# Kernel optimization log

Measured on AMD Instinct MI355X. Metric: run time of the kernel, lower is better.

Reference implementation:

```python
import jax, jax.numpy as jnp
import numpy as np

# Mamba block dims (config: d_model=1024, expand=2, d_state=16, d_conv=4, dt_rank=auto)
D_MODEL = 1024
D_INNER = 2048
D_STATE = 16
D_CONV = 4
DT_RANK = 64
B_SZ = 2
SEQ = 2048
EPS = 1e-5
DT_MIN, DT_MAX, DT_FLOOR = 0.001, 0.1, 1e-4


def setup_inputs() -> dict:
    key = jax.random.key(0)
    ks = jax.random.split(key, 8)
    s = 0.02  # initializer_range
    # dt_proj bias init: inverse-softplus of dt sampled log-uniform in [dt_min, dt_max]
    dt = jnp.exp(jax.random.uniform(ks[6], (D_INNER,)) * (np.log(DT_MAX) - np.log(DT_MIN)) + np.log(DT_MIN))
    dt = jnp.clip(dt, DT_FLOOR, None)
    inv_dt = dt + jnp.log(-jnp.expm1(-dt))
    A_init = jnp.broadcast_to(jnp.arange(1, D_STATE + 1, dtype=jnp.float32), (D_INNER, D_STATE))
    return {
        "hidden_states": jax.random.normal(ks[0], (B_SZ, SEQ, D_MODEL), jnp.float32),
        "norm_weight": jnp.ones((D_MODEL,), jnp.float32),
        "in_proj_w": jax.random.normal(ks[1], (2 * D_INNER, D_MODEL), jnp.float32) * s,
        "conv_w": jax.random.normal(ks[2], (D_INNER, 1, D_CONV), jnp.float32) * s,
        "conv_b": jnp.zeros((D_INNER,), jnp.float32),
        "x_proj_w": jax.random.normal(ks[3], (DT_RANK + 2 * D_STATE, D_INNER), jnp.float32) * s,
        "dt_proj_w": jax.random.normal(ks[4], (D_INNER, DT_RANK), jnp.float32) * s,
        "dt_proj_b": inv_dt,
        "A_log": jnp.log(A_init),
        "D": jnp.ones((D_INNER,), jnp.float32),
        "out_proj_w": jax.random.normal(ks[5], (D_MODEL, D_INNER), jnp.float32) * s,
    }


def reference(hidden_states, norm_weight, in_proj_w, conv_w, conv_b, x_proj_w,
              dt_proj_w, dt_proj_b, A_log, D, out_proj_w):
    residual = hidden_states
    # RMSNorm
    h = hidden_states * jax.lax.rsqrt(jnp.mean(hidden_states * hidden_states, -1, keepdims=True) + EPS)
    h = h * norm_weight
    # input projection -> x (ssm branch) and z (gate)
    xz = h @ in_proj_w.T                      # [B, L, 2*d_inner]
    x, z = jnp.split(xz, 2, axis=-1)
    # causal depthwise conv over time
    xc = x.transpose(0, 2, 1)                 # [B, d_inner, L]
    xc = jax.lax.conv_general_dilated(
        xc, conv_w, window_strides=(1,), padding=[(D_CONV - 1, 0)],
        feature_group_count=D_INNER, dimension_numbers=("NCH", "OIH", "NCH"))
    xc = xc + conv_b[None, :, None]
    x = jax.nn.silu(xc.transpose(0, 2, 1))    # [B, L, d_inner]
    # data-dependent SSM params
    dbl = x @ x_proj_w.T                      # [B, L, dt_rank + 2*d_state]
    dt_r = dbl[..., :DT_RANK]
    Bm = dbl[..., DT_RANK:DT_RANK + D_STATE]  # [B, L, N]
    Cm = dbl[..., DT_RANK + D_STATE:]         # [B, L, N]
    dt = jax.nn.softplus(dt_r @ dt_proj_w.T + dt_proj_b)  # [B, L, d_inner]
    A = -jnp.exp(A_log)                       # [d_inner, N], negative

    def step(hstate, inputs):
        x_t, dt_t, B_t, C_t = inputs          # [B,d],[B,d],[B,N],[B,N]
        dA = jnp.exp(dt_t[..., None] * A)     # [B, d, N]
        hstate = hstate * dA + (dt_t * x_t)[..., None] * B_t[:, None, :]
        y_t = jnp.einsum("bdn,bn->bd", hstate, C_t)
        return hstate, y_t

    xs = (x.transpose(1, 0, 2), dt.transpose(1, 0, 2),
          Bm.transpose(1, 0, 2), Cm.transpose(1, 0, 2))
    h0 = jnp.zeros((hidden_states.shape[0], D_INNER, D_STATE), x.dtype)
    _, ys = jax.lax.scan(step, h0, xs)        # ys: [L, B, d_inner]
    y = ys.transpose(1, 0, 2) + x * D
    y = y * jax.nn.silu(z)                    # gated output
    return y @ out_proj_w.T + residual
```

## Files before the change

kernel.cpp:

```cpp
#include <hip/hip_runtime.h>
#include <math.h>

#define D_MODEL 1024
#define D_INNER 2048
#define D_STATE 16
#define D_CONV  4
#define DT_RANK 64
#define B_SZ    2
#define SEQ     2048
#define NTOK    (B_SZ*SEQ)
#define DBL_N   (DT_RANK + 2*D_STATE)
#define CHUNK   64
#define NCHUNK  (SEQ/CHUNK)

typedef __attribute__((ext_vector_type(8))) short short8;
typedef __attribute__((ext_vector_type(4))) float f32x4;

__device__ __forceinline__ unsigned short f2bf(float f) {
    union { float f; unsigned int u; } v; v.f = f;
    unsigned int r = v.u + 0x7fff + ((v.u >> 16) & 1);
    return (unsigned short)(r >> 16);
}
__device__ __forceinline__ float bf2f(unsigned short u) {
    union { unsigned int u; float f; } v; v.u = ((unsigned int)u) << 16;
    return v.f;
}

__global__ __launch_bounds__(256) void rmsnorm_kernel(
    const float* __restrict__ h, const float* __restrict__ w, unsigned short* __restrict__ out)
{
    int tok = blockIdx.x;
    const float4* row = (const float4*)(h + (size_t)tok * D_MODEL);
    float4 v = row[threadIdx.x];
    float ss = v.x*v.x + v.y*v.y + v.z*v.z + v.w*v.w;
    #pragma unroll
    for (int off = 32; off >= 1; off >>= 1) ss += __shfl_down(ss, off, 64);
    __shared__ float red[4];
    int wave = threadIdx.x >> 6, lane = threadIdx.x & 63;
    if (lane == 0) red[wave] = ss;
    __syncthreads();
    float tot = red[0] + red[1] + red[2] + red[3];
    float scale = rsqrtf(tot * (1.0f / D_MODEL) + 1e-5f);
    float4 wv = ((const float4*)w)[threadIdx.x];
    ushort4 o;
    o.x = f2bf(v.x * scale * wv.x);
    o.y = f2bf(v.y * scale * wv.y);
    o.z = f2bf(v.z * scale * wv.z);
    o.w = f2bf(v.w * scale * wv.w);
    ((ushort4*)(out + (size_t)tok * D_MODEL))[threadIdx.x] = o;
}

__global__ __launch_bounds__(256) void cast_bf16_kernel(
    const float4* __restrict__ in, ushort4* __restrict__ out, int n4)
{
    int i = blockIdx.x * 256 + threadIdx.x;
    if (i < n4) {
        float4 v = in[i];
        ushort4 o; o.x = f2bf(v.x); o.y = f2bf(v.y); o.z = f2bf(v.z); o.w = f2bf(v.w);
        out[i] = o;
    }
}

__global__ __launch_bounds__(256) void mfma_gemm_kernel(
    const unsigned short* __restrict__ A, int lda,
    const unsigned short* __restrict__ W, int ldw,
    float* __restrict__ C, int ldc,
    unsigned short* __restrict__ Cbf, int ldcbf,
    int kLen, int Nmax,
    const float* __restrict__ bias,
    const float* __restrict__ add, int ldadd,
    int act, size_t segStride)
{
    __shared__ __align__(16) unsigned short As[128 * 32];
    __shared__ __align__(16) unsigned short Bs[128 * 32];
    const int bm = blockIdx.y * 128;
    const int bn = blockIdx.x * 128;
    const int kBeg = blockIdx.z * kLen;
    const int tid = threadIdx.x;
    const int lane = tid & 63;
    const int wave = tid >> 6;
    const int wm = (wave >> 1) * 64;
    const int wn = (wave & 1) * 64;
    const int frow = lane & 15;
    const int quad = lane >> 4;
    const int sw = (frow >> 1) & 3;

    if (C) C += blockIdx.z * segStride;

    f32x4 acc[4][4];
    #pragma unroll
    for (int i = 0; i < 4; ++i)
        #pragma unroll
        for (int j = 0; j < 4; ++j)
            acc[i][j] = (f32x4){0.f, 0.f, 0.f, 0.f};

    for (int k0 = kBeg; k0 < kBeg + kLen; k0 += 32) {
        __syncthreads();
        #pragma unroll
        for (int i = 0; i < 2; ++i) {
            int q = (wave * 2 + i) * 64 + lane;
            int r = q >> 2, cl = q & 3;
            int cg = cl ^ ((r >> 1) & 3);
            const unsigned short* ga = A + (size_t)(bm + r) * lda + k0 + cg * 8;
            const unsigned short* gb = W + (size_t)(bn + r) * ldw + k0 + cg * 8;
            __builtin_amdgcn_global_load_lds(
                (const __attribute__((address_space(1))) void*)ga,
                (__attribute__((address_space(3))) void*)(As + (wave * 2 + i) * 512),
                16, 0, 0);
            __builtin_amdgcn_global_load_lds(
                (const __attribute__((address_space(1))) void*)gb,
                (__attribute__((address_space(3))) void*)(Bs + (wave * 2 + i) * 512),
                16, 0, 0);
        }
        __syncthreads();
        short8 af[4], bf[4];
        #pragma unroll
        for (int i = 0; i < 4; ++i)
            af[i] = *(const short8*)&As[(wm + i * 16 + frow) * 32 + (quad ^ sw) * 8];
        #pragma unroll
        for (int j = 0; j < 4; ++j)
            bf[j] = *(const short8*)&Bs[(wn + j * 16 + frow) * 32 + (quad ^ sw) * 8];
        #pragma unroll
        for (int i = 0; i < 4; ++i)
            #pragma unroll
            for (int j = 0; j < 4; ++j)
                acc[i][j] = __builtin_amdgcn_mfma_f32_16x16x32_bf16(
                    af[i], bf[j], acc[i][j], 0, 0, 0);
    }

    #pragma unroll
    for (int i = 0; i < 4; ++i) {
        #pragma unroll
        for (int r = 0; r < 4; ++r) {
            int row = bm + wm + i * 16 + quad * 4 + r;
            #pragma unroll
            for (int j = 0; j < 4; ++j) {
                int col = bn + wn + j * 16 + frow;
                if (col < Nmax) {
                    float v = acc[i][j][r];
                    if (bias) v += bias[col];
                    if (act == 1) v = (v > 20.0f) ? v : log1pf(__expf(v));
                    if (add) v += add[(size_t)row * ldadd + col];
                    if (C)   C[(size_t)row * ldc + col] = v;
                    if (Cbf) Cbf[(size_t)row * ldcbf + col] = f2bf(v);
                }
            }
        }
    }
}

__global__ __launch_bounds__(256) void reduce_xproj_kernel(
    const float* __restrict__ part, float* __restrict__ dbl,
    unsigned short* __restrict__ dtr)
{
    const int N = NTOK * DBL_N;
    int idx = blockIdx.x * 256 + threadIdx.x;
    if (idx >= N) return;
    float s = part[idx] + part[idx + N] + part[idx + 2 * N] + part[idx + 3 * N];
    dbl[idx] = s;
    unsigned int col = (unsigned int)idx % DBL_N;
    if (col < DT_RANK) {
        unsigned int tok = (unsigned int)idx / DBL_N;
        dtr[(size_t)tok * DT_RANK + col] = f2bf(s);
    }
}

__global__ __launch_bounds__(256) void conv_silu_kernel(
    const unsigned short* __restrict__ xz, const float* __restrict__ cw,
    const float* __restrict__ cb, unsigned short* __restrict__ out_bf)
{
    int idx = blockIdx.x * 256 + threadIdx.x;
    int d = idx & (D_INNER - 1);
    int t = (idx >> 11) & (SEQ - 1);
    int b = idx >> 22;
    const unsigned short* xcol = xz + (size_t)b * SEQ * (2 * D_INNER) + d;
    float w0 = cw[d * 4 + 0], w1 = cw[d * 4 + 1], w2 = cw[d * 4 + 2], w3 = cw[d * 4 + 3];
    float acc = cb[d];
    if (t >= 3) acc = fmaf(bf2f(xcol[(size_t)(t - 3) * (2 * D_INNER)]), w0, acc);
    if (t >= 2) acc = fmaf(bf2f(xcol[(size_t)(t - 2) * (2 * D_INNER)]), w1, acc);
    if (t >= 1) acc = fmaf(bf2f(xcol[(size_t)(t - 1) * (2 * D_INNER)]), w2, acc);
    acc = fmaf(bf2f(xcol[(size_t)t * (2 * D_INNER)]), w3, acc);
    float sig = 1.0f / (1.0f + __expf(-acc));
    out_bf[(size_t)(b * SEQ + t) * D_INNER + d] = f2bf(acc * sig);
}

__global__ __launch_bounds__(256) void scan_phase1_kernel(
    const float* __restrict__ dtb, const unsigned short* __restrict__ xconv,
    const float* __restrict__ dbl, const float* __restrict__ A_log,
    float* __restrict__ sum_a, float* __restrict__ sum_h)
{
    const int d = blockIdx.y * 256 + threadIdx.x;
    const int c = blockIdx.x;
    const int b = blockIdx.z;
    const int t0 = c * CHUNK;

    float An[D_STATE];
    bool fast = true;
    #pragma unroll
    for (int n = 0; n < D_STATE; ++n) {
        An[n] = -__expf(A_log[d * D_STATE + n]);
        fast = fast && (fabsf(An[n] + (float)(n + 1)) < 2e-3f);
    }
    const float* dt_p = dtb + ((size_t)b * SEQ + t0) * D_INNER + d;
    const unsigned short* x_p = xconv + ((size_t)b * SEQ + t0) * D_INNER + d;
    const float* Brow = dbl + ((size_t)b * SEQ + t0) * DBL_N + DT_RANK;

    float h[D_STATE];
    #pragma unroll
    for (int n = 0; n < D_STATE; ++n) h[n] = 0.f;
    float sumdt = 0.f;

    if (fast) {
        for (int t = 0; t < CHUNK; ++t) {
            float dt = dt_p[(size_t)t * D_INNER];
            float xv = bf2f(x_p[(size_t)t * D_INNER]);
            const float4* B4 = (const float4*)(Brow + (size_t)t * DBL_N);
            float4 b0 = B4[0], b1 = B4[1], b2 = B4[2], b3 = B4[3];
            float Bv[16] = {b0.x,b0.y,b0.z,b0.w, b1.x,b1.y,b1.z,b1.w,
                            b2.x,b2.y,b2.z,b2.w, b3.x,b3.y,b3.z,b3.w};
            sumdt += dt;
            float e1 = __expf(-dt);
            float dtx = dt * xv;
            float ea = 1.f;
            #pragma unroll
            for (int n = 0; n < D_STATE; ++n) {
                ea *= e1;
                h[n] = fmaf(h[n], ea, dtx * Bv[n]);
            }
        }
    } else {
        for (int t = 0; t < CHUNK; ++t) {
            float dt = dt_p[(size_t)t * D_INNER];
            float xv = bf2f(x_p[(size_t)t * D_INNER]);
            const float4* B4 = (const float4*)(Brow + (size_t)t * DBL_N);
            float4 b0 = B4[0], b1 = B4[1], b2 = B4[2], b3 = B4[3];
            float Bv[16] = {b0.x,b0.y,b0.z,b0.w, b1.x,b1.y,b1.z,b1.w,
                            b2.x,b2.y,b2.z,b2.w, b3.x,b3.y,b3.z,b3.w};
            sumdt += dt;
            float dtx = dt * xv;
            #pragma unroll
            for (int n = 0; n < D_STATE; ++n) {
                float ea = __expf(dt * An[n]);
                h[n] = fmaf(h[n], ea, dtx * Bv[n]);
            }
        }
    }

    float a[D_STATE];
    if (fast) {
        float E = __expf(-sumdt);
        float ea = 1.f;
        #pragma unroll
        for (int n = 0; n < D_STATE; ++n) { ea *= E; a[n] = ea; }
    } else {
        #pragma unroll
        for (int n = 0; n < D_STATE; ++n) a[n] = __expf(An[n] * sumdt);
    }
    size_t base = (((size_t)b * D_INNER + d) * NCHUNK + c) * D_STATE;
    #pragma unroll
    for (int i = 0; i < 4; ++i) {
        ((float4*)(sum_a + base))[i] = (float4){a[4*i], a[4*i+1], a[4*i+2], a[4*i+3]};
        ((float4*)(sum_h + base))[i] = (float4){h[4*i], h[4*i+1], h[4*i+2], h[4*i+3]};
    }
}

__global__ __launch_bounds__(256) void scan_carry_kernel(
    const float* __restrict__ sum_a, float* __restrict__ sum_h)
{
    size_t g = (size_t)blockIdx.x * 256 + threadIdx.x;
    size_t bd = g >> 4;
    int n = (int)(g & 15);
    size_t base = bd * NCHUNK * D_STATE + n;
    float hh = 0.f;
    for (int c = 0; c < NCHUNK; ++c) {
        size_t idx = base + (size_t)c * D_STATE;
        float a = sum_a[idx];
        float hp = sum_h[idx];
        sum_h[idx] = hh;
        hh = fmaf(hh, a, hp);
    }
}

__global__ __launch_bounds__(256) void scan_phase3_kernel(
    const float* __restrict__ dtb, const unsigned short* __restrict__ xconv,
    const unsigned short* __restrict__ xz, const float* __restrict__ dbl,
    const float* __restrict__ A_log, const float* __restrict__ Dvec,
    const float* __restrict__ hinit, unsigned short* __restrict__ y)
{
    const int d = blockIdx.y * 256 + threadIdx.x;
    const int c = blockIdx.x;
    const int b = blockIdx.z;
    const int t0 = c * CHUNK;

    float An[D_STATE];
    bool fast = true;
    #pragma unroll
    for (int n = 0; n < D_STATE; ++n) {
        An[n] = -__expf(A_log[d * D_STATE + n]);
        fast = fast && (fabsf(An[n] + (float)(n + 1)) < 2e-3f);
    }
    const float Dd = Dvec[d];
    const float* dt_p = dtb + ((size_t)b * SEQ + t0) * D_INNER + d;
    const unsigned short* x_p = xconv + ((size_t)b * SEQ + t0) * D_INNER + d;
    const unsigned short* z_p = xz + ((size_t)b * SEQ + t0) * (2 * D_INNER) + D_INNER + d;
    const float* Brow = dbl + ((size_t)b * SEQ + t0) * DBL_N + DT_RANK;
    unsigned short* y_p = y + ((size_t)b * SEQ + t0) * D_INNER + d;

    size_t base = (((size_t)b * D_INNER + d) * NCHUNK + c) * D_STATE;
    float h[D_STATE];
    #pragma unroll
    for (int i = 0; i < 4; ++i) {
        float4 hv = ((const float4*)(hinit + base))[i];
        h[4*i] = hv.x; h[4*i+1] = hv.y; h[4*i+2] = hv.z; h[4*i+3] = hv.w;
    }

    if (fast) {
        for (int t = 0; t < CHUNK; ++t) {
            float dt = dt_p[(size_t)t * D_INNER];
            float xv = bf2f(x_p[(size_t)t * D_INNER]);
            const float4* B4 = (const float4*)(Brow + (size_t)t * DBL_N);
            float4 b0 = B4[0], b1 = B4[1], b2 = B4[2], b3 = B4[3];
            float4 c0 = B4[4], c1 = B4[5], c2 = B4[6], c3 = B4[7];
            float Bv[16] = {b0.x,b0.y,b0.z,b0.w, b1.x,b1.y,b1.z,b1.w,
                            b2.x,b2.y,b2.z,b2.w, b3.x,b3.y,b3.z,b3.w};
            float Cv[16] = {c0.x,c0.y,c0.z,c0.w, c1.x,c1.y,c1.z,c1.w,
                            c2.x,c2.y,c2.z,c2.w, c3.x,c3.y,c3.z,c3.w};
            float e1 = __expf(-dt);
            float dtx = dt * xv;
            float ea = 1.f, yy = 0.f;
            #pragma unroll
            for (int n = 0; n < D_STATE; ++n) {
                ea *= e1;
                h[n] = fmaf(h[n], ea, dtx * Bv[n]);
                yy = fmaf(h[n], Cv[n], yy);
            }
            float zv = bf2f(z_p[(size_t)t * (2 * D_INNER)]);
            float sig = 1.0f / (1.0f + __expf(-zv));
            y_p[(size_t)t * D_INNER] = f2bf((yy + xv * Dd) * (zv * sig));
        }
    } else {
        for (int t = 0; t < CHUNK; ++t) {
            float dt = dt_p[(size_t)t * D_INNER];
            float xv = bf2f(x_p[(size_t)t * D_INNER]);
            const float4* B4 = (const float4*)(Brow + (size_t)t * DBL_N);
            float4 b0 = B4[0], b1 = B4[1], b2 = B4[2], b3 = B4[3];
            float4 c0 = B4[4], c1 = B4[5], c2 = B4[6], c3 = B4[7];
            float Bv[16] = {b0.x,b0.y,b0.z,b0.w, b1.x,b1.y,b1.z,b1.w,
                            b2.x,b2.y,b2.z,b2.w, b3.x,b3.y,b3.z,b3.w};
            float Cv[16] = {c0.x,c0.y,c0.z,c0.w, c1.x,c1.y,c1.z,c1.w,
                            c2.x,c2.y,c2.z,c2.w, c3.x,c3.y,c3.z,c3.w};
            float dtx = dt * xv;
            float yy = 0.f;
            #pragma unroll
            for (int n = 0; n < D_STATE; ++n) {
                float ea = __expf(dt * An[n]);
                h[n] = fmaf(h[n], ea, dtx * Bv[n]);
                yy = fmaf(h[n], Cv[n], yy);
            }
            float zv = bf2f(z_p[(size_t)t * (2 * D_INNER)]);
            float sig = 1.0f / (1.0f + __expf(-zv));
            y_p[(size_t)t * D_INNER] = f2bf((yy + xv * Dd) * (zv * sig));
        }
    }
}

extern "C" void kernel_launch(void* const* d_in, const int* in_sizes, int n_in,
                              void* d_out, int out_size, void* d_ws, size_t ws_size,
                              hipStream_t stream) {
    const float* hs        = (const float*)d_in[0];
    const float* norm_w    = (const float*)d_in[1];
    const float* in_proj_w = (const float*)d_in[2];
    const float* conv_w    = (const float*)d_in[3];
    const float* conv_b    = (const float*)d_in[4];
    const float* x_proj_w  = (const float*)d_in[5];
    const float* dt_proj_w = (const float*)d_in[6];
    const float* dt_proj_b = (const float*)d_in[7];
    const float* A_log     = (const float*)d_in[8];
    const float* Dvec      = (const float*)d_in[9];
    const float* out_proj_w= (const float*)d_in[10];
    float* out = (float*)d_out;

    float* wsf      = (float*)d_ws;
    float* dbl      = wsf;
    float* dbl_part = dbl      + (size_t)393216;
    float* dtb      = dbl_part + (size_t)1572864;
    float* sum_a    = dtb      + (size_t)8388608;
    float* sum_h    = sum_a    + (size_t)2097152;
    unsigned short* xz_bf    = (unsigned short*)(sum_h + 2097152);
    unsigned short* xconv_bf = xz_bf    + (size_t)16777216;
    unsigned short* hnorm_bf = xconv_bf + (size_t)8388608;
    unsigned short* ybuf_bf  = hnorm_bf + (size_t)4194304;
    unsigned short* wi_bf    = ybuf_bf  + (size_t)8388608;
    unsigned short* wo_bf    = wi_bf    + (size_t)4194304;
    unsigned short* wx_bf    = wo_bf    + (size_t)2097152;
    unsigned short* wdt_bf   = wx_bf    + (size_t)262144;
    unsigned short* dtr_bf   = wdt_bf   + (size_t)131072;

    cast_bf16_kernel<<<(2 * D_INNER * D_MODEL / 4 + 255) / 256, 256, 0, stream>>>(
        (const float4*)in_proj_w, (ushort4*)wi_bf, 2 * D_INNER * D_MODEL / 4);
    cast_bf16_kernel<<<(D_MODEL * D_INNER / 4 + 255) / 256, 256, 0, stream>>>(
        (const float4*)out_proj_w, (ushort4*)wo_bf, D_MODEL * D_INNER / 4);
    cast_bf16_kernel<<<(DBL_N * D_INNER / 4 + 255) / 256, 256, 0, stream>>>(
        (const float4*)x_proj_w, (ushort4*)wx_bf, DBL_N * D_INNER / 4);
    cast_bf16_kernel<<<(D_INNER * DT_RANK / 4 + 255) / 256, 256, 0, stream>>>(
        (const float4*)dt_proj_w, (ushort4*)wdt_bf, D_INNER * DT_RANK / 4);

    rmsnorm_kernel<<<NTOK, 256, 0, stream>>>(hs, norm_w, hnorm_bf);
    mfma_gemm_kernel<<<dim3((2 * D_INNER) / 128, NTOK / 128), 256, 0, stream>>>(
        hnorm_bf, D_MODEL, wi_bf, D_MODEL, nullptr, 0, xz_bf, 2 * D_INNER,
        D_MODEL, 2 * D_INNER, nullptr, nullptr, 0, 0, 0);
    conv_silu_kernel<<<(NTOK * D_INNER) / 256, 256, 0, stream>>>(
        xz_bf, conv_w, conv_b, xconv_bf);
    mfma_gemm_kernel<<<dim3(1, NTOK / 128, 4), 256, 0, stream>>>(
        xconv_bf, D_INNER, wx_bf, D_INNER, dbl_part, DBL_N, nullptr, 0,
        D_INNER / 4, DBL_N, nullptr, nullptr, 0, 0, (size_t)NTOK * DBL_N);
    reduce_xproj_kernel<<<(NTOK * DBL_N + 255) / 256, 256, 0, stream>>>(
        dbl_part, dbl, dtr_bf);
    mfma_gemm_kernel<<<dim3(D_INNER / 128, NTOK / 128), 256, 0, stream>>>(
        dtr_bf, DT_RANK, wdt_bf, DT_RANK, dtb, D_INNER, nullptr, 0,
        DT_RANK, D_INNER, dt_proj_b, nullptr, 0, 1, 0);
    scan_phase1_kernel<<<dim3(NCHUNK, D_INNER / 256, B_SZ), 256, 0, stream>>>(
        dtb, xconv_bf, dbl, A_log, sum_a, sum_h);
    scan_carry_kernel<<<(B_SZ * D_INNER * D_STATE) / 256, 256, 0, stream>>>(sum_a, sum_h);
    scan_phase3_kernel<<<dim3(NCHUNK, D_INNER / 256, B_SZ), 256, 0, stream>>>(
        dtb, xconv_bf, xz_bf, dbl, A_log, Dvec, sum_h, ybuf_bf);
    mfma_gemm_kernel<<<dim3(D_MODEL / 128, NTOK / 128), 256, 0, stream>>>(
        ybuf_bf, D_INNER, wo_bf, D_INNER, out, D_MODEL, nullptr, 0,
        D_INNER, D_MODEL, nullptr, hs, D_MODEL, 0, 0);
}
```

Baseline: 403.2 us.

## Merge weight casts into one launch, vectorize GEMM epilogue, drop LDS swizzle

```diff
diff --git a/kernel.cpp b/kernel.cpp
--- a/kernel.cpp
+++ b/kernel.cpp
@@ -50,15 +50,22 @@
     ((ushort4*)(out + (size_t)tok * D_MODEL))[threadIdx.x] = o;
 }
 
-__global__ __launch_bounds__(256) void cast_bf16_kernel(
-    const float4* __restrict__ in, ushort4* __restrict__ out, int n4)
+__global__ __launch_bounds__(256) void cast4_kernel(
+    const float4* __restrict__ s0, ushort4* __restrict__ d0, int n0,
+    const float4* __restrict__ s1, ushort4* __restrict__ d1, int n1,
+    const float4* __restrict__ s2, ushort4* __restrict__ d2, int n2,
+    const float4* __restrict__ s3, ushort4* __restrict__ d3, int n3)
 {
     int i = blockIdx.x * 256 + threadIdx.x;
-    if (i < n4) {
-        float4 v = in[i];
-        ushort4 o; o.x = f2bf(v.x); o.y = f2bf(v.y); o.z = f2bf(v.z); o.w = f2bf(v.w);
-        out[i] = o;
-    }
+    const float4* s; ushort4* d;
+    if (i < n0) { s = s0; d = d0; }
+    else if ((i -= n0) < n1) { s = s1; d = d1; }
+    else if ((i -= n1) < n2) { s = s2; d = d2; }
+    else if ((i -= n2) < n3) { s = s3; d = d3; }
+    else return;
+    float4 v = s[i];
+    ushort4 o; o.x = f2bf(v.x); o.y = f2bf(v.y); o.z = f2bf(v.z); o.w = f2bf(v.w);
+    d[i] = o;
 }
 
 __global__ __launch_bounds__(256) void mfma_gemm_kernel(
@@ -83,7 +90,6 @@
     const int wn = (wave & 1) * 64;
     const int frow = lane & 15;
     const int quad = lane >> 4;
-    const int sw = (frow >> 1) & 3;
 
     if (C) C += blockIdx.z * segStride;
 
@@ -100,9 +106,8 @@
         for (int i = 0; i < 2; ++i) {
             int q = (wave * 2 + i) * 64 + lane;
             int r = q >> 2, cl = q & 3;
-            int cg = cl ^ ((r >> 1) & 3);
-            const unsigned short* ga = A + (size_t)(bm + r) * lda + k0 + cg * 8;
-            const unsigned short* gb = W + (size_t)(bn + r) * ldw + k0 + cg * 8;
+            const unsigned short* ga = A + (size_t)(bm + r) * lda + k0 + cl * 8;
+            const unsigned short* gb = W + (size_t)(bn + r) * ldw + k0 + cl * 8;
             __builtin_amdgcn_global_load_lds(
                 (const __attribute__((address_space(1))) void*)ga,
                 (__attribute__((address_space(3))) void*)(As + (wave * 2 + i) * 512),
@@ -116,33 +121,46 @@
         short8 af[4], bf[4];
         #pragma unroll
         for (int i = 0; i < 4; ++i)
-            af[i] = *(const short8*)&As[(wm + i * 16 + frow) * 32 + (quad ^ sw) * 8];
+            af[i] = *(const short8*)&As[(wm + i * 16 + frow) * 32 + quad * 8];
         #pragma unroll
         for (int j = 0; j < 4; ++j)
-            bf[j] = *(const short8*)&Bs[(wn + j * 16 + frow) * 32 + (quad ^ sw) * 8];
+            bf[j] = *(const short8*)&Bs[(wn + j * 16 + frow) * 32 + quad * 8];
         #pragma unroll
         for (int i = 0; i < 4; ++i)
             #pragma unroll
             for (int j = 0; j < 4; ++j)
                 acc[i][j] = __builtin_amdgcn_mfma_f32_16x16x32_bf16(
-                    af[i], bf[j], acc[i][j], 0, 0, 0);
+                    bf[j], af[i], acc[i][j], 0, 0, 0);
     }
 
     #pragma unroll
     for (int i = 0; i < 4; ++i) {
-        #pragma unroll
-        for (int r = 0; r < 4; ++r) {
-            int row = bm + wm + i * 16 + quad * 4 + r;
-            #pragma unroll
-            for (int j = 0; j < 4; ++j) {
-                int col = bn + wn + j * 16 + frow;
-                if (col < Nmax) {
-                    float v = acc[i][j][r];
-                    if (bias) v += bias[col];
-                    if (act == 1) v = (v > 20.0f) ? v : log1pf(__expf(v));
-                    if (add) v += add[(size_t)row * ldadd + col];
-                    if (C)   C[(size_t)row * ldc + col] = v;
-                    if (Cbf) Cbf[(size_t)row * ldcbf + col] = f2bf(v);
+        int row = bm + wm + i * 16 + frow;
+        #pragma unroll
+        for (int j = 0; j < 4; ++j) {
+            int col = bn + wn + j * 16 + quad * 4;
+            if (col < Nmax) {
+                f32x4 v = acc[i][j];
+                if (bias) {
+                    float4 bv = *(const float4*)&bias[col];
+                    v[0] += bv.x; v[1] += bv.y; v[2] += bv.z; v[3] += bv.w;
+                }
+                if (act == 1) {
+                    #pragma unroll
+                    for (int r = 0; r < 4; ++r)
+                        v[r] = (v[r] > 20.0f) ? v[r] : log1pf(__expf(v[r]));
+                }
+                if (add) {
+                    float4 av = *(const float4*)&add[(size_t)row * ldadd + col];
+                    v[0] += av.x; v[1] += av.y; v[2] += av.z; v[3] += av.w;
+                }
+                if (C) {
+                    float4 o = {v[0], v[1], v[2], v[3]};
+                    *(float4*)&C[(size_t)row * ldc + col] = o;
+                }
+                if (Cbf) {
+                    ushort4 o = {f2bf(v[0]), f2bf(v[1]), f2bf(v[2]), f2bf(v[3])};
+                    *(ushort4*)&Cbf[(size_t)row * ldcbf + col] = o;
                 }
             }
         }
@@ -396,14 +414,18 @@
     unsigned short* wdt_bf   = wx_bf    + (size_t)262144;
     unsigned short* dtr_bf   = wdt_bf   + (size_t)131072;
 
-    cast_bf16_kernel<<<(2 * D_INNER * D_MODEL / 4 + 255) / 256, 256, 0, stream>>>(
-        (const float4*)in_proj_w, (ushort4*)wi_bf, 2 * D_INNER * D_MODEL / 4);
-    cast_bf16_kernel<<<(D_MODEL * D_INNER / 4 + 255) / 256, 256, 0, stream>>>(
-        (const float4*)out_proj_w, (ushort4*)wo_bf, D_MODEL * D_INNER / 4);
-    cast_bf16_kernel<<<(DBL_N * D_INNER / 4 + 255) / 256, 256, 0, stream>>>(
-        (const float4*)x_proj_w, (ushort4*)wx_bf, DBL_N * D_INNER / 4);
-    cast_bf16_kernel<<<(D_INNER * DT_RANK / 4 + 255) / 256, 256, 0, stream>>>(
-        (const float4*)dt_proj_w, (ushort4*)wdt_bf, D_INNER * DT_RANK / 4);
+    {
+        int n0 = 2 * D_INNER * D_MODEL / 4;
+        int n1 = D_MODEL * D_INNER / 4;
+        int n2 = DBL_N * D_INNER / 4;
+        int n3 = D_INNER * DT_RANK / 4;
+        int tot = n0 + n1 + n2 + n3;
+        cast4_kernel<<<(tot + 255) / 256, 256, 0, stream>>>(
+            (const float4*)in_proj_w,  (ushort4*)wi_bf,  n0,
+            (const float4*)out_proj_w, (ushort4*)wo_bf,  n1,
+            (const float4*)x_proj_w,   (ushort4*)wx_bf,  n2,
+            (const float4*)dt_proj_w,  (ushort4*)wdt_bf, n3);
+    }
 
     rmsnorm_kernel<<<NTOK, 256, 0, stream>>>(hs, norm_w, hnorm_bf);
     mfma_gemm_kernel<<<dim3((2 * D_INNER) / 128, NTOK / 128), 256, 0, stream>>>(
```

Result: faster. 376.6 us (-6.6%).
